# Performance work log

Hardware: AMD Instinct MI355X
Metric: run time of the kernel (lower is better)

The kernel has to match this reference:

```python
import jax, jax.numpy as jnp
import numpy as np

CONF_THRESH = 0.25
IOU_THRESH = 0.45
MAX_DET = 300          # max_per_img
MIN_DET = 1            # min_per_img
PRE_NMS_TOPK = 512     # fixed candidate pool per image (jit-friendly stand-in for conf filtering)
MAX_WH = 7680.0        # class-offset trick for class-aware NMS (as in yolov5)
ANCHORS_PER_CELL = 3   # matches `ids // 3` in the wrapper


def setup_inputs() -> dict:
    key = jax.random.key(0)
    k1, k2, k3, k4 = jax.random.split(key, 4)
    bs, n, nc = 64, 25200, 3
    cxcy = jax.random.uniform(k1, (bs, n, 2), dtype=jnp.float32) * 640.0
    wh = jax.random.uniform(k2, (bs, n, 2), dtype=jnp.float32) * 64.0 + 2.0
    obj = jax.random.uniform(k3, (bs, n, 1), dtype=jnp.float32)
    cls = jax.random.uniform(k4, (bs, n, nc), dtype=jnp.float32)
    pred = jnp.concatenate([cxcy, wh, obj, cls], axis=-1)  # [bs, n, 5+nc]
    return {"pred": pred}


def reference(pred):
    """Confidence scoring + class-aware greedy NMS (yolov5-style), fixed-shape outputs."""
    bs = pred.shape[0]
    K = PRE_NMS_TOPK
    obj = pred[..., 4]                                   # [bs, n]
    cls_scores = obj[..., None] * pred[..., 5:]          # conf = obj * cls (multi_label=False)
    best = jnp.max(cls_scores, axis=-1)                  # [bs, n]
    cls_id = jnp.argmax(cls_scores, axis=-1)             # [bs, n]

    # pre-NMS candidate selection (sorted by score desc)
    topv, topi = jax.lax.top_k(best, K)                  # [bs, K]
    xywh = jnp.take_along_axis(pred[..., :4], topi[..., None], axis=1)
    boxes = jnp.concatenate([xywh[..., :2] - xywh[..., 2:] * 0.5,
                             xywh[..., :2] + xywh[..., 2:] * 0.5], axis=-1)  # xyxy
    cid = jnp.take_along_axis(cls_id, topi, axis=1)
    conf_ok = topv > CONF_THRESH

    # class offset so boxes of different classes never overlap
    ob = boxes + (cid.astype(boxes.dtype) * MAX_WH)[..., None]

    # pairwise IoU per image: [bs, K, K]
    area = (ob[..., 2] - ob[..., 0]) * (ob[..., 3] - ob[..., 1])
    lt = jnp.maximum(ob[:, :, None, :2], ob[:, None, :, :2])
    rb = jnp.minimum(ob[:, :, None, 2:], ob[:, None, :, 2:])
    whi = jnp.clip(rb - lt, 0.0)
    inter = whi[..., 0] * whi[..., 1]
    iou = inter / (area[:, :, None] + area[:, None, :] - inter + 1e-7)

    upper = jnp.arange(K)[None, :] > jnp.arange(K)[:, None]  # j > i (candidates sorted by score)

    def body(i, suppressed):
        keep_i = jnp.logical_not(suppressed[:, i])           # [bs]
        new_sup = keep_i[:, None] & (iou[:, i, :] > IOU_THRESH) & upper[i]
        return suppressed | new_sup

    suppressed = jax.lax.fori_loop(0, K, body, jnp.zeros((bs, K), dtype=bool))
    keep = jnp.logical_not(suppressed)

    # enforce min_per_img: the first MIN_DET kept boxes survive even below conf_thresh
    rank = jnp.cumsum(keep.astype(jnp.int32), axis=1)
    valid = keep & (conf_ok | (rank <= MIN_DET))

    # pack top MAX_DET surviving detections (padded, fixed shape)
    sel = jnp.where(valid, topv, -1.0)
    sv, si = jax.lax.top_k(sel, MAX_DET)                  # [bs, MAX_DET]
    out_valid = sv > -0.5
    out_boxes = jnp.take_along_axis(boxes, si[..., None], axis=1)
    out_scores = jnp.take_along_axis(topv, si, axis=1)
    out_cls = jnp.take_along_axis(cid, si, axis=1)
    out_ids = jnp.take_along_axis(topi, si, axis=1) // ANCHORS_PER_CELL  # matches `ids // 3`
    out_boxes = jnp.where(out_valid[..., None], out_boxes, 0.0)
    out_scores = jnp.where(out_valid, out_scores, 0.0)
    return out_boxes, out_scores, out_cls, out_ids, out_valid
```

## Files before the change

### kernel.cpp

```cpp
#include <hip/hip_runtime.h>
#include <cstdint>
#include <cstddef>

#define BS      64
#define NPRED   25200
#define KTOP    512
#define MAXDET  300
#define NBINS   4096
#define CAP     1024
#define NTHR    1024
#define CONF_T  0.25f
#define IOU_T   0.45f
#define MAXWH   7680.0f
#define MSTRIDE 18
#define NITER   25

__device__ __forceinline__ unsigned long long shflx64(unsigned long long v, int m) {
  unsigned lo = __shfl_xor((unsigned)(v & 0xffffffffull), m, 64);
  unsigned hi = __shfl_xor((unsigned)(v >> 32), m, 64);
  return (((unsigned long long)hi) << 32) | lo;
}

__device__ __forceinline__ float scoreOf(const float4& q) {
  return fmaxf(q.x * q.y, fmaxf(q.x * q.z, q.x * q.w));
}

__global__ __launch_bounds__(NTHR) void yolo_k(const float* __restrict__ pred,
                                               float* __restrict__ out) {
  __shared__ unsigned long long keysL[CAP];
  __shared__ __align__(16) unsigned int maskA[KTOP * MSTRIDE];
  __shared__ float ox0[KTOP], oy0[KTOP], ox1[KTOP], oy1[KTOP], areaL[KTOP];
  __shared__ float bx0[KTOP], bx1[KTOP], bx2[KTOP], bx3[KTOP];
  __shared__ float svL[KTOP]; __shared__ int siL[KTOP]; __shared__ int cidL[KTOP];
  __shared__ unsigned int supW[16];
  __shared__ unsigned int wtot[16];
  __shared__ int woff[8];
  __shared__ int cutoff_s, cnt_s, nvalid_s;

  unsigned int* hist = maskA;

  const int tid = threadIdx.x;
  const int lane = tid & 63;
  const int wid = tid >> 6;
  const int img = blockIdx.x;
  const float* __restrict__ base = pred + (size_t)img * (NPRED * 8);

  if (tid == 0) cnt_s = 0;

  for (int b = tid; b < NBINS; b += NTHR) hist[b] = 0u;
  __syncthreads();
  float sc[NITER];
#pragma unroll
  for (int it = 0; it < NITER; ++it) {
    const int e = tid + (it << 10);
    float m = -1.0f;
    if (e < NPRED) {
      const float4 q = *reinterpret_cast<const float4*>(base + (size_t)e * 8 + 4);
      m = scoreOf(q);
      int b = (int)(m * (float)NBINS);
      b = min(max(b, 0), NBINS - 1);
      atomicAdd(&hist[b], 1u);
    }
    sc[it] = m;
  }
  __syncthreads();
  const uint4 h = *reinterpret_cast<const uint4*>(hist + (tid << 2));
  const unsigned h0 = h.x, h1 = h.y, h2 = h.z, h3 = h.w;

  unsigned g = h0 + h1 + h2 + h3;
  unsigned s = g;
#pragma unroll
  for (int d = 1; d < 64; d <<= 1) {
    unsigned o = __shfl_down(s, d, 64);
    if (lane + d < 64) s += o;
  }
  if (lane == 0) wtot[wid] = s;
  __syncthreads();
  if (tid < 16) {
    unsigned t = wtot[tid];
#pragma unroll
    for (int d = 1; d < 16; d <<= 1) {
      unsigned o = __shfl_down(t, d, 64);
      if (tid + d < 16) t += o;
    }
    wtot[tid] = t;
  }
  __syncthreads();
  unsigned S = s + ((wid < 15) ? wtot[wid + 1] : 0u);
  if (S >= KTOP && (S - g) < KTOP) {
    unsigned acc = S - g;
    int cut;
    acc += h3;
    if (acc >= KTOP) cut = 4 * tid + 3;
    else {
      acc += h2;
      if (acc >= KTOP) cut = 4 * tid + 2;
      else {
        acc += h1;
        if (acc >= KTOP) cut = 4 * tid + 1;
        else cut = 4 * tid;
      }
    }
    cutoff_s = cut;
  }
  __syncthreads();
  const int cutoff = cutoff_s;

#pragma unroll
  for (int it = 0; it < NITER; ++it) {
    const int e = tid + (it << 10);
    if (e < NPRED) {
      float m = sc[it];
      int b = (int)(m * (float)NBINS);
      b = min(max(b, 0), NBINS - 1);
      if (b >= cutoff) {
        int p = atomicAdd(&cnt_s, 1);
        if (p < CAP) {
          keysL[p] = (((unsigned long long)__float_as_uint(m)) << 32)
                   | (unsigned)(0x7FFFFFFF - e);
        }
      }
    }
  }
  __syncthreads();
  const int cnt = min(cnt_s, CAP);
  unsigned long long key = (tid < cnt) ? keysL[tid] : 0ull;

  for (int k = 2; k <= CAP; k <<= 1) {
    for (int j = k >> 1; j > 0; j >>= 1) {
      unsigned long long p;
      if (j >= 64) {
        __syncthreads();
        keysL[tid] = key;
        __syncthreads();
        p = keysL[tid ^ j];
      } else {
        p = shflx64(key, j);
      }
      bool lower = ((tid & j) == 0);
      bool descR = ((tid & k) == 0);
      bool takeMax = (lower == descR);
      bool pGreater = (p > key);
      key = (takeMax == pGreater) ? p : key;
    }
  }

  if (tid < KTOP) {
    int gi = 0x7FFFFFFF - (int)(unsigned)(key & 0xffffffffull);
    if ((unsigned)gi >= NPRED) gi = 0;
    float v = __uint_as_float((unsigned)(key >> 32));
    const float4 a = *reinterpret_cast<const float4*>(base + (size_t)gi * 8);
    const float4 q = *reinterpret_cast<const float4*>(base + (size_t)gi * 8 + 4);
    float p0 = q.x * q.y, p1 = q.x * q.z, p2 = q.x * q.w;
    float m = fmaxf(p0, fmaxf(p1, p2));
    int c = (p0 == m) ? 0 : ((p1 == m) ? 1 : 2);
    float x0 = a.x - a.z * 0.5f;
    float y0 = a.y - a.w * 0.5f;
    float x1 = a.x + a.z * 0.5f;
    float y1 = a.y + a.w * 0.5f;
    float co = (float)c * MAXWH;
    bx0[tid] = x0; bx1[tid] = y0; bx2[tid] = x1; bx3[tid] = y1;
    float o0 = x0 + co, o1 = y0 + co, o2 = x1 + co, o3 = y1 + co;
    ox0[tid] = o0; oy0[tid] = o1; ox1[tid] = o2; oy1[tid] = o3;
    areaL[tid] = (o2 - o0) * (o3 - o1);
    cidL[tid] = c;
    svL[tid] = v; siL[tid] = gi;
  }
  __syncthreads();
  for (int w = tid; w < KTOP * MSTRIDE; w += NTHR) maskA[w] = 0u;
  __syncthreads();

  {
    for (int jb = 0; jb < 8; ++jb) {
      const int j = (jb << 6) + lane;
      const float jx0 = ox0[j], jy0 = oy0[j], jx1 = ox1[j], jy1 = oy1[j];
      const float ja = areaL[j];
      const int ilim = (jb + 1) << 6;
      for (int i = wid; i < ilim; i += 16) {
        const float ix0 = ox0[i], iy0 = oy0[i], ix1 = ox1[i], iy1 = oy1[i];
        const float ia = areaL[i];
        float xx0 = fmaxf(ix0, jx0);
        float yy0 = fmaxf(iy0, jy0);
        float xx1 = fminf(ix1, jx1);
        float yy1 = fminf(iy1, jy1);
        float iw = fmaxf(xx1 - xx0, 0.0f);
        float ih = fmaxf(yy1 - yy0, 0.0f);
        float inter = iw * ih;
        float denom = ia + ja - inter + 1e-7f;
        bool sup = (inter > IOU_T * denom) && (j > i);
        unsigned long long bal = __ballot(sup);
        if (lane == 0) {
          *reinterpret_cast<unsigned long long*>(maskA + i * MSTRIDE + (jb << 1)) = bal;
        }
      }
    }
  }
  __syncthreads();

  if (tid < 16) {
    unsigned sst = 0u;
    for (int c = 0; c < KTOP / 16; ++c) {
      const int rb = c * 16;
      const int wi = rb >> 5;
      const int b0 = rb & 31;
      unsigned myrow[16], diag[16];
#pragma unroll
      for (int r = 0; r < 16; ++r) {
        myrow[r] = maskA[(rb + r) * MSTRIDE + tid];
        diag[r]  = maskA[(rb + r) * MSTRIDE + wi];
      }
      unsigned wcur = __shfl(sst, wi, 64);
#pragma unroll
      for (int r = 0; r < 16; ++r) {
        if (!((wcur >> (b0 + r)) & 1u)) { sst |= myrow[r]; wcur |= diag[r]; }
      }
    }
    supW[tid] = sst;
  }
  __syncthreads();

  bool keep = false;
  float score = 0.0f;
  if (tid < KTOP) {
    keep = !((supW[tid >> 5] >> (tid & 31)) & 1u);
    score = svL[tid];
  }
  unsigned long long balK = __ballot(keep);
  int wpre = __popcll(balK & ((1ull << lane) - 1ull));
  if (lane == 63 && wid < 8) wtot[wid] = (unsigned)(wpre + (keep ? 1 : 0));
  __syncthreads();
  if (tid == 0) {
    int a = 0;
    for (int w = 0; w < 8; ++w) { woff[w] = a; a += (int)wtot[w]; }
  }
  __syncthreads();
  bool valid = false;
  if (tid < KTOP) {
    int rank = woff[wid] + wpre + (keep ? 1 : 0);
    valid = keep && ((score > CONF_T) || (rank <= 1));
  }
  __syncthreads();
  unsigned long long balV = __ballot(valid);
  int vpre = __popcll(balV & ((1ull << lane) - 1ull));
  if (lane == 63 && wid < 8) wtot[wid] = (unsigned)(vpre + (valid ? 1 : 0));
  __syncthreads();
  if (tid == 0) {
    int a = 0;
    for (int w = 0; w < 8; ++w) { woff[w] = a; a += (int)wtot[w]; }
    nvalid_s = a;
  }
  __syncthreads();
  if (tid < KTOP) {
    int vs = woff[wid] + vpre + (valid ? 1 : 0);
    int nvalid = nvalid_s;
    int pos = valid ? (vs - 1) : (nvalid + tid - vs);
    if (pos < MAXDET) {
      const int SB = BS * MAXDET;
      float* outBoxes  = out;
      float* outScores = out + (size_t)SB * 4;
      float* outCls    = outScores + SB;
      float* outIds    = outCls + SB;
      float* outValid  = outIds + SB;
      size_t row = (size_t)img * MAXDET + pos;
      if (valid) {
        outBoxes[row * 4 + 0] = bx0[tid];
        outBoxes[row * 4 + 1] = bx1[tid];
        outBoxes[row * 4 + 2] = bx2[tid];
        outBoxes[row * 4 + 3] = bx3[tid];
        outScores[row] = score;
      } else {
        outBoxes[row * 4 + 0] = 0.0f;
        outBoxes[row * 4 + 1] = 0.0f;
        outBoxes[row * 4 + 2] = 0.0f;
        outBoxes[row * 4 + 3] = 0.0f;
        outScores[row] = 0.0f;
      }
      outCls[row]   = (float)cidL[tid];
      outIds[row]   = (float)(siL[tid] / 3);
      outValid[row] = valid ? 1.0f : 0.0f;
    }
  }
}

extern "C" void kernel_launch(void* const* d_in, const int* in_sizes, int n_in,
                              void* d_out, int out_size, void* d_ws, size_t ws_size,
                              hipStream_t stream) {
  (void)in_sizes; (void)n_in; (void)out_size; (void)d_ws; (void)ws_size;
  const float* pred = (const float*)d_in[0];
  float* out = (float*)d_out;
  yolo_k<<<BS, NTHR, 0, stream>>>(pred, out);
}
```

Before: 134.5 us.

## Register-cache j boxes and write full mask rows, dropping mask zeroing pass

The IoU mask loop now loads all eight j-box blocks per lane into registers once and iterates rows i per wavefront, computing all column blocks for a row and writing the full 16-word row with one cooperative store from 16 lanes. This removes the separate pass that zeroed the mask (and its barrier) and the shared-memory area array, since areas are recomputed in registers. It raises register pressure from the per-lane arrays in a 1024-thread block, and the reordering changes which wave handles which rows.

New measurement: 129.7 us. -3.5%, faster.

```diff
diff --git a/kernel.cpp b/kernel.cpp
--- a/kernel.cpp
+++ b/kernel.cpp
@@ -29,7 +29,7 @@
                                                float* __restrict__ out) {
   __shared__ unsigned long long keysL[CAP];
   __shared__ __align__(16) unsigned int maskA[KTOP * MSTRIDE];
-  __shared__ float ox0[KTOP], oy0[KTOP], ox1[KTOP], oy1[KTOP], areaL[KTOP];
+  __shared__ float ox0[KTOP], oy0[KTOP], ox1[KTOP], oy1[KTOP];
   __shared__ float bx0[KTOP], bx1[KTOP], bx2[KTOP], bx3[KTOP];
   __shared__ float svL[KTOP]; __shared__ int siL[KTOP]; __shared__ int cidL[KTOP];
   __shared__ unsigned int supW[16];
@@ -160,39 +160,51 @@
     float y1 = a.y + a.w * 0.5f;
     float co = (float)c * MAXWH;
     bx0[tid] = x0; bx1[tid] = y0; bx2[tid] = x1; bx3[tid] = y1;
-    float o0 = x0 + co, o1 = y0 + co, o2 = x1 + co, o3 = y1 + co;
-    ox0[tid] = o0; oy0[tid] = o1; ox1[tid] = o2; oy1[tid] = o3;
-    areaL[tid] = (o2 - o0) * (o3 - o1);
+    ox0[tid] = x0 + co; oy0[tid] = y0 + co; ox1[tid] = x1 + co; oy1[tid] = y1 + co;
     cidL[tid] = c;
     svL[tid] = v; siL[tid] = gi;
   }
   __syncthreads();
-  for (int w = tid; w < KTOP * MSTRIDE; w += NTHR) maskA[w] = 0u;
-  __syncthreads();
 
   {
+    float jx0[8], jy0[8], jx1[8], jy1[8], jA[8];
+#pragma unroll
     for (int jb = 0; jb < 8; ++jb) {
       const int j = (jb << 6) + lane;
-      const float jx0 = ox0[j], jy0 = oy0[j], jx1 = ox1[j], jy1 = oy1[j];
-      const float ja = areaL[j];
-      const int ilim = (jb + 1) << 6;
-      for (int i = wid; i < ilim; i += 16) {
-        const float ix0 = ox0[i], iy0 = oy0[i], ix1 = ox1[i], iy1 = oy1[i];
-        const float ia = areaL[i];
-        float xx0 = fmaxf(ix0, jx0);
-        float yy0 = fmaxf(iy0, jy0);
-        float xx1 = fminf(ix1, jx1);
-        float yy1 = fminf(iy1, jy1);
-        float iw = fmaxf(xx1 - xx0, 0.0f);
-        float ih = fmaxf(yy1 - yy0, 0.0f);
-        float inter = iw * ih;
-        float denom = ia + ja - inter + 1e-7f;
-        bool sup = (inter > IOU_T * denom) && (j > i);
-        unsigned long long bal = __ballot(sup);
-        if (lane == 0) {
-          *reinterpret_cast<unsigned long long*>(maskA + i * MSTRIDE + (jb << 1)) = bal;
+      jx0[jb] = ox0[j]; jy0[jb] = oy0[j];
+      jx1[jb] = ox1[j]; jy1[jb] = oy1[j];
+      jA[jb] = (jx1[jb] - jx0[jb]) * (jy1[jb] - jy0[jb]);
+    }
+    for (int t = 0; t < KTOP / 16; ++t) {
+      const int i = wid + (t << 4);
+      const float ix0 = ox0[i], iy0 = oy0[i], ix1 = ox1[i], iy1 = oy1[i];
+      const float ia = (ix1 - ix0) * (iy1 - iy0);
+      const int jb0 = i >> 6;
+      unsigned long long b[8];
+#pragma unroll
+      for (int jb = 0; jb < 8; ++jb) {
+        b[jb] = 0ull;
+        if (jb >= jb0) {
+          const int j = (jb << 6) + lane;
+          float xx0 = fmaxf(ix0, jx0[jb]);
+          float yy0 = fmaxf(iy0, jy0[jb]);
+          float xx1 = fminf(ix1, jx1[jb]);
+          float yy1 = fminf(iy1, jy1[jb]);
+          float iw = fmaxf(xx1 - xx0, 0.0f);
+          float ih = fmaxf(yy1 - yy0, 0.0f);
+          float inter = iw * ih;
+          float denom = ia + jA[jb] - inter + 1e-7f;
+          bool sup = (inter > IOU_T * denom) && (j > i);
+          b[jb] = __ballot(sup);
         }
       }
+      unsigned w = 0u;
+#pragma unroll
+      for (int jb = 0; jb < 8; ++jb) {
+        unsigned piece = (lane & 1) ? (unsigned)(b[jb] >> 32) : (unsigned)b[jb];
+        w = ((lane >> 1) == jb) ? piece : w;
+      }
+      if (lane < 16) maskA[i * MSTRIDE + lane] = w;
     }
   }
   __syncthreads();
```
